# Kernel tuning notes

Measured on AMD Instinct MI355X. Metric: run time of the kernel, lower is better.

The kernel has to match this reference:

```python
import jax, jax.numpy as jnp
import numpy as np

N_NODES = 50000
N_EDGES = 800000
IN_SIZE = 128
NUM_HEADS = 8
HEAD_DIM = IN_SIZE // NUM_HEADS  # qk/val head dim = 16


def setup_inputs() -> dict:
    key = jax.random.key(0)
    ks = jax.random.split(key, 16)
    d = IN_SIZE
    lim = 1.0 / np.sqrt(d)
    inp = {
        "in_feats": jax.random.normal(ks[0], (N_NODES, d), jnp.float32),
        "struc_feats": jax.random.normal(ks[1], (N_NODES, d), jnp.float32),
        "edge_weights": jax.random.uniform(ks[2], (N_EDGES,), jnp.float32),
        "ln_scale": jnp.ones((d,), jnp.float32),
        "ln_bias": jnp.zeros((d,), jnp.float32),
        "Ws": jax.random.uniform(ks[3], (d, d), jnp.float32, -lim, lim),
        "bs": jnp.zeros((d,), jnp.float32),
        "Wq": jax.random.uniform(ks[4], (d, d), jnp.float32, -lim, lim),
        "bq": jnp.zeros((d,), jnp.float32),
        "Wk": jax.random.uniform(ks[5], (d, d), jnp.float32, -lim, lim),
        "bk": jnp.zeros((d,), jnp.float32),
        "Wv": jax.random.uniform(ks[6], (d, d), jnp.float32, -lim, lim),
        "bv": jnp.zeros((d,), jnp.float32),
        "Wo": jax.random.uniform(ks[7], (d, d), jnp.float32, -lim, lim),
        "edge_ids": jax.random.randint(ks[8], (2, N_EDGES), 0, N_NODES, jnp.int64)
        if jax.config.jax_enable_x64 else jax.random.randint(ks[8], (2, N_EDGES), 0, N_NODES, jnp.int32),
    }
    return inp


def _layer_norm(x, scale, bias, eps=1e-5):
    mu = jnp.mean(x, axis=-1, keepdims=True)
    var = jnp.var(x, axis=-1, keepdims=True)
    return (x - mu) * jax.lax.rsqrt(var + eps) * scale + bias


def reference(in_feats, struc_feats, edge_weights, ln_scale, ln_bias,
              Ws, bs, Wq, bq, Wk, bk, Wv, bv, Wo, edge_ids):
    N = in_feats.shape[0]
    H, hd = NUM_HEADS, HEAD_DIM

    delta = _layer_norm(in_feats, ln_scale, ln_bias)           # pre-norm
    delta = jax.nn.gelu(delta, approximate=False)               # pre-activation (exact GELU, torch default)
    delta_struc = delta + struc_feats @ Ws.T + bs               # struc_proj add

    qry = (delta_struc @ Wq.T + bq) / np.sqrt(hd)                # [N, qk]
    keyf = delta_struc @ Wk.T + bk                               # [N, qk]
    val = delta @ Wv.T + bv                                      # [N, val]

    src, dst = edge_ids[0], edge_ids[1]                          # out[src] += A[src,dst] * val[dst]
    qe = qry[src].reshape(-1, H, hd)                             # [E, H, hd]
    ke = keyf[dst].reshape(-1, H, hd)                            # [E, H, hd]
    attn = jax.nn.sigmoid(jnp.sum(qe * ke, axis=-1))             # [E, H]
    attn = edge_weights[:, None] * attn

    msgs = attn[:, :, None] * val[dst].reshape(-1, H, hd)        # [E, H, hd]
    agg = jax.ops.segment_sum(msgs.reshape(-1, H * hd), src, num_segments=N)  # [N, val]

    out = agg @ Wo.T                                             # out_proj (no bias)
    return in_feats + out                                        # skip connection
```

## Files before the change

### kernel.cpp

```cpp
#include <hip/hip_runtime.h>
#include <math.h>

#define NF 128

typedef __attribute__((ext_vector_type(8))) short short8;
typedef __attribute__((ext_vector_type(4))) float floatx4;

__device__ __forceinline__ unsigned short f2bf(float f) {
    union { float x; unsigned int i; } c; c.x = f;
    unsigned int r = c.i + 0x7fffu + ((c.i >> 16) & 1u);
    return (unsigned short)(r >> 16);
}
__device__ __forceinline__ float bf2f(unsigned short u) {
    union { unsigned int i; float x; } c; c.i = ((unsigned int)u) << 16;
    return c.x;
}
__device__ __forceinline__ void unpack8(uint4 u, float* f) {
    union { unsigned int i; float x; } c;
    c.i = u.x << 16;          f[0] = c.x;
    c.i = u.x & 0xffff0000u;  f[1] = c.x;
    c.i = u.y << 16;          f[2] = c.x;
    c.i = u.y & 0xffff0000u;  f[3] = c.x;
    c.i = u.z << 16;          f[4] = c.x;
    c.i = u.z & 0xffff0000u;  f[5] = c.x;
    c.i = u.w << 16;          f[6] = c.x;
    c.i = u.w & 0xffff0000u;  f[7] = c.x;
}
__device__ __forceinline__ ushort4 pack4(float a, float b, float c, float d) {
    ushort4 h; h.x = f2bf(a); h.y = f2bf(b); h.z = f2bf(c); h.w = f2bf(d);
    return h;
}

__global__ __launch_bounds__(256) void wconv_hist_kernel(
    const float* __restrict__ a, const float* __restrict__ b,
    const float* __restrict__ c, const float* __restrict__ d,
    const float* __restrict__ e, unsigned short* __restrict__ o,
    const int* __restrict__ eid, int* __restrict__ cnt,
    int* __restrict__ rank, int E)
{
    int blk = blockIdx.x;
    if (blk < 320) {
        int i = blk * 256 + threadIdx.x;
        int w = i >> 14, j = i & 16383;
        const float* p = (w == 0) ? a : (w == 1) ? b : (w == 2) ? c : (w == 3) ? d : e;
        o[i] = f2bf(p[j]);
    } else {
        int i = (blk - 320) * 256 + threadIdx.x;
        if (i < E) rank[i] = atomicAdd(&cnt[eid[i]], 1);
    }
}

__global__ __launch_bounds__(256) void scan1_kernel(
    const int* __restrict__ cnt, int* __restrict__ bsum, int n)
{
    int base = blockIdx.x * 1024;
    int s = 0;
    #pragma unroll
    for (int p = 0; p < 4; ++p) {
        int i = base + (int)threadIdx.x + p * 256;
        if (i < n) s += cnt[i];
    }
    #pragma unroll
    for (int m = 1; m <= 32; m <<= 1) s += __shfl_xor(s, m, 64);
    __shared__ int ws_[4];
    int wid = threadIdx.x >> 6;
    if ((threadIdx.x & 63) == 0) ws_[wid] = s;
    __syncthreads();
    if (threadIdx.x == 0) bsum[blockIdx.x] = ws_[0] + ws_[1] + ws_[2] + ws_[3];
}

__global__ __launch_bounds__(256) void scan3_kernel(
    const int* __restrict__ cnt, const int* __restrict__ bsum,
    int* __restrict__ row_start, int n, int nb)
{
    __shared__ int base_off;
    int tid = threadIdx.x, lane = tid & 63, wid = tid >> 6;
    if (tid == 0) {
        int a = 0;
        for (int j = 0; j < (int)blockIdx.x; ++j) a += bsum[j];
        base_off = a;
        if ((int)blockIdx.x == nb - 1) {
            int tot = a;
            for (int j = blockIdx.x; j < nb; ++j) tot += bsum[j];
            row_start[n] = tot;
        }
    }
    int base = blockIdx.x * 1024;
    int v[4]; int s = 0;
    #pragma unroll
    for (int p = 0; p < 4; ++p) {
        int i = base + tid * 4 + p;
        v[p] = (i < n) ? cnt[i] : 0;
        s += v[p];
    }
    int ss = s;
    #pragma unroll
    for (int off = 1; off < 64; off <<= 1) {
        int t = __shfl_up(ss, off, 64);
        if (lane >= off) ss += t;
    }
    __shared__ int wsum[4];
    if (lane == 63) wsum[wid] = ss;
    __syncthreads();
    int woff = 0;
    for (int j = 0; j < wid; ++j) woff += wsum[j];
    int a = base_off + woff + (ss - s);
    #pragma unroll
    for (int p = 0; p < 4; ++p) {
        int i = base + tid * 4 + p;
        if (i < n) { row_start[i] = a; a += v[p]; }
    }
}

__global__ __launch_bounds__(256) void scatter_prep_kernel(
    const int* __restrict__ eid, const float* __restrict__ ew,
    const int* __restrict__ row_start, const int* __restrict__ rank,
    int2* __restrict__ edata, int E, int sb,
    const float* __restrict__ in_feats, const float* __restrict__ gamma,
    const float* __restrict__ beta, unsigned short* __restrict__ deltab, int M)
{
    int blk = blockIdx.x;
    if (blk < sb) {
        int i = blk * 256 + threadIdx.x;
        if (i < E) {
            int src = eid[i];
            int pos = row_start[src] + rank[i];
            edata[pos] = make_int2(eid[E + i], __float_as_int(ew[i]));
        }
        return;
    }
    int li = (blk - sb) * 256 + threadIdx.x;
    int row = li >> 2, t4 = li & 3;
    if (row >= M) return;
    size_t rbase = (size_t)row * NF;

    const float4* ip = (const float4*)(in_feats + rbase) + t4 * 8;
    float4 xf[8];
    #pragma unroll
    for (int p = 0; p < 8; ++p) xf[p] = ip[p];
    float s = 0.f, sq = 0.f;
    #pragma unroll
    for (int p = 0; p < 8; ++p) {
        s  += xf[p].x + xf[p].y + xf[p].z + xf[p].w;
        sq += xf[p].x * xf[p].x + xf[p].y * xf[p].y
            + xf[p].z * xf[p].z + xf[p].w * xf[p].w;
    }
    s  += __shfl_xor(s, 1, 64);  s  += __shfl_xor(s, 2, 64);
    sq += __shfl_xor(sq, 1, 64); sq += __shfl_xor(sq, 2, 64);
    float mu = s * (1.0f / 128.0f);
    float var = sq * (1.0f / 128.0f) - mu * mu;
    float rstd = rsqrtf(var + 1e-5f);

    const float4* gp = (const float4*)gamma + t4 * 8;
    const float4* bp = (const float4*)beta + t4 * 8;
    uint dreg[16];
    #pragma unroll
    for (int p = 0; p < 8; ++p) {
        float4 g4 = gp[p], b4 = bp[p];
        float o0 = (xf[p].x - mu) * rstd * g4.x + b4.x;
        float o1 = (xf[p].y - mu) * rstd * g4.y + b4.y;
        float o2 = (xf[p].z - mu) * rstd * g4.z + b4.z;
        float o3 = (xf[p].w - mu) * rstd * g4.w + b4.w;
        o0 = 0.5f * o0 * (1.0f + erff(o0 * 0.70710678118654752f));
        o1 = 0.5f * o1 * (1.0f + erff(o1 * 0.70710678118654752f));
        o2 = 0.5f * o2 * (1.0f + erff(o2 * 0.70710678118654752f));
        o3 = 0.5f * o3 * (1.0f + erff(o3 * 0.70710678118654752f));
        ushort4 h = pack4(o0, o1, o2, o3);
        dreg[p * 2]     = (uint)h.x | ((uint)h.y << 16);
        dreg[p * 2 + 1] = (uint)h.z | ((uint)h.w << 16);
    }
    uint4* od = (uint4*)(deltab + rbase + t4 * 32);
    #pragma unroll
    for (int q = 0; q < 4; ++q)
        od[q] = make_uint4(dreg[q*4], dreg[q*4+1], dreg[q*4+2], dreg[q*4+3]);
}

__global__ __launch_bounds__(256) void gemm_dv_kernel(
    const float* __restrict__ struc, const unsigned short* __restrict__ deltab,
    const unsigned short* __restrict__ Wall, const float* __restrict__ bs,
    const float* __restrict__ bv, unsigned short* __restrict__ dstrb,
    unsigned short* __restrict__ kvb, int M, int nt)
{
    __shared__ unsigned short Wl[128][136];
    __shared__ unsigned short Cst[64][136];

    int tid = threadIdx.x;
    int y = blockIdx.y;
    int lane = tid & 63, w = tid >> 6, lg = lane & 15, quad = lane >> 4;

    const unsigned short* Wg = Wall + ((y == 0) ? 0 : 3 * 16384);
    const float* bias = (y == 0) ? bs : bv;
    unsigned short* outg = (y == 0) ? dstrb : (kvb + NF);
    int ostride = (y == 0) ? NF : 2 * NF;

    {
        const uint4* g = (const uint4*)Wg;
        #pragma unroll
        for (int p = 0; p < 8; ++p) {
            int idx = tid + p * 256;
            *(uint4*)&Wl[idx >> 4][(idx & 15) * 8] = g[idx];
        }
    }
    float br[8];
    #pragma unroll
    for (int t = 0; t < 8; ++t) br[t] = bias[t * 16 + lg];
    __syncthreads();

    for (int tile = blockIdx.x; tile < nt; tile += gridDim.x) {
        int m0 = tile * 64;
        int am = m0 + w * 16 + lg;
        size_t rb = (size_t)(am < M ? am : 0) * NF;

        short8 af[4];
        if (y == 0) {
            const float4* sp = (const float4*)(struc + rb);
            #pragma unroll
            for (int ks = 0; ks < 4; ++ks) {
                float4 f0 = sp[ks * 8 + quad * 2];
                float4 f1 = sp[ks * 8 + quad * 2 + 1];
                ushort4 h0 = pack4(f0.x, f0.y, f0.z, f0.w);
                ushort4 h1 = pack4(f1.x, f1.y, f1.z, f1.w);
                uint4 pk = make_uint4((uint)h0.x | ((uint)h0.y << 16),
                                      (uint)h0.z | ((uint)h0.w << 16),
                                      (uint)h1.x | ((uint)h1.y << 16),
                                      (uint)h1.z | ((uint)h1.w << 16));
                af[ks] = *(short8*)&pk;
            }
        } else {
            const unsigned short* arow = deltab + rb + quad * 8;
            #pragma unroll
            for (int ks = 0; ks < 4; ++ks) af[ks] = *(const short8*)(arow + ks * 32);
        }

        floatx4 acc[8];
        #pragma unroll
        for (int t = 0; t < 8; ++t) acc[t] = (floatx4){0.f, 0.f, 0.f, 0.f};
        #pragma unroll
        for (int ks = 0; ks < 4; ++ks) {
            #pragma unroll
            for (int t = 0; t < 8; ++t) {
                short8 b = *(const short8*)&Wl[t * 16 + lg][ks * 32 + quad * 8];
                acc[t] = __builtin_amdgcn_mfma_f32_16x16x32_bf16(af[ks], b, acc[t], 0, 0, 0);
            }
        }

        if (y == 0) {
            #pragma unroll
            for (int t = 0; t < 8; ++t) {
                int col = t * 16 + lg;
                #pragma unroll
                for (int r = 0; r < 4; ++r) {
                    int gm = m0 + w * 16 + quad * 4 + r;
                    float dadd = bf2f(deltab[(size_t)(gm < M ? gm : 0) * NF + col]);
                    Cst[w * 16 + quad * 4 + r][col] = f2bf(acc[t][r] + br[t] + dadd);
                }
            }
        } else {
            #pragma unroll
            for (int t = 0; t < 8; ++t) {
                int col = t * 16 + lg;
                #pragma unroll
                for (int r = 0; r < 4; ++r)
                    Cst[w * 16 + quad * 4 + r][col] = f2bf(acc[t][r] + br[t]);
            }
        }
        #pragma unroll
        for (int p = 0; p < 4; ++p) {
            int idx = lane + p * 64;
            int row = w * 16 + (idx >> 4), c16 = idx & 15;
            int gm = m0 + row;
            if (gm < M)
                *(uint4*)(outg + (size_t)gm * ostride + c16 * 8) = *(const uint4*)&Cst[row][c16 * 8];
        }
    }
}

__global__ __launch_bounds__(256) void gemm_qk_kernel(
    const unsigned short* __restrict__ dstrb, const unsigned short* __restrict__ Wall,
    const float* __restrict__ bq, const float* __restrict__ bk,
    unsigned short* __restrict__ qb, unsigned short* __restrict__ kvb,
    int M, int nt)
{
    __shared__ unsigned short Wl[128][136];
    __shared__ unsigned short Cst[64][136];

    int tid = threadIdx.x;
    int y = blockIdx.y;
    int lane = tid & 63, w = tid >> 6, lg = lane & 15, quad = lane >> 4;

    const unsigned short* Wg = Wall + (y + 1) * 16384;
    const float* bias = (y == 0) ? bq : bk;
    float scale = (y == 0) ? 0.25f : 1.0f;
    unsigned short* outg = (y == 0) ? qb : kvb;
    int ostride = (y == 0) ? NF : 2 * NF;

    {
        const uint4* g = (const uint4*)Wg;
        #pragma unroll
        for (int p = 0; p < 8; ++p) {
            int idx = tid + p * 256;
            *(uint4*)&Wl[idx >> 4][(idx & 15) * 8] = g[idx];
        }
    }
    float br[8];
    #pragma unroll
    for (int t = 0; t < 8; ++t) br[t] = bias[t * 16 + lg] * scale;
    __syncthreads();

    for (int tile = blockIdx.x; tile < nt; tile += gridDim.x) {
        int m0 = tile * 64;
        int am = m0 + w * 16 + lg;
        const unsigned short* arow = dstrb + (size_t)(am < M ? am : 0) * NF + quad * 8;

        floatx4 acc[8];
        #pragma unroll
        for (int t = 0; t < 8; ++t) acc[t] = (floatx4){0.f, 0.f, 0.f, 0.f};
        short8 af[4];
        #pragma unroll
        for (int ks = 0; ks < 4; ++ks) af[ks] = *(const short8*)(arow + ks * 32);
        #pragma unroll
        for (int ks = 0; ks < 4; ++ks) {
            #pragma unroll
            for (int t = 0; t < 8; ++t) {
                short8 b = *(const short8*)&Wl[t * 16 + lg][ks * 32 + quad * 8];
                acc[t] = __builtin_amdgcn_mfma_f32_16x16x32_bf16(af[ks], b, acc[t], 0, 0, 0);
            }
        }
        #pragma unroll
        for (int t = 0; t < 8; ++t) {
            int col = t * 16 + lg;
            #pragma unroll
            for (int r = 0; r < 4; ++r)
                Cst[w * 16 + quad * 4 + r][col] = f2bf(acc[t][r] * scale + br[t]);
        }
        #pragma unroll
        for (int p = 0; p < 4; ++p) {
            int idx = lane + p * 64;
            int row = w * 16 + (idx >> 4), c16 = idx & 15;
            int gm = m0 + row;
            if (gm < M)
                *(uint4*)(outg + (size_t)gm * ostride + c16 * 8) = *(const uint4*)&Cst[row][c16 * 8];
        }
    }
}

__global__ __launch_bounds__(256) void gemm_out_kernel(
    const unsigned short* __restrict__ Xb, const unsigned short* __restrict__ Wb,
    const float* __restrict__ addf, float* __restrict__ Y, int M, int nt)
{
    __shared__ unsigned short Wl[128][136];
    int tid = threadIdx.x;
    int lane = tid & 63, w = tid >> 6, lg = lane & 15, quad = lane >> 4;

    {
        const uint4* g = (const uint4*)Wb;
        #pragma unroll
        for (int p = 0; p < 8; ++p) {
            int idx = tid + p * 256;
            *(uint4*)&Wl[idx >> 4][(idx & 15) * 8] = g[idx];
        }
    }
    __syncthreads();

    for (int tile = blockIdx.x; tile < nt; tile += gridDim.x) {
        int m0 = tile * 64;
        int am = m0 + w * 16 + lg;
        const unsigned short* arow = Xb + (size_t)(am < M ? am : 0) * NF + quad * 8;

        floatx4 acc[8];
        #pragma unroll
        for (int t = 0; t < 8; ++t) acc[t] = (floatx4){0.f, 0.f, 0.f, 0.f};
        short8 af[4];
        #pragma unroll
        for (int ks = 0; ks < 4; ++ks) af[ks] = *(const short8*)(arow + ks * 32);
        #pragma unroll
        for (int ks = 0; ks < 4; ++ks) {
            #pragma unroll
            for (int t = 0; t < 8; ++t) {
                short8 b = *(const short8*)&Wl[t * 16 + lg][ks * 32 + quad * 8];
                acc[t] = __builtin_amdgcn_mfma_f32_16x16x32_bf16(af[ks], b, acc[t], 0, 0, 0);
            }
        }
        #pragma unroll
        for (int t = 0; t < 8; ++t) {
            int col = t * 16 + lg;
            #pragma unroll
            for (int r = 0; r < 4; ++r) {
                int gm = m0 + w * 16 + quad * 4 + r;
                if (gm >= M) continue;
                size_t off = (size_t)gm * NF + col;
                Y[off] = acc[t][r] + addf[off];
            }
        }
    }
}

__global__ __launch_bounds__(256) void aggregate_kernel(
    const unsigned short* __restrict__ Q, const unsigned short* __restrict__ kvb,
    const int* __restrict__ row_start, const int2* __restrict__ edata,
    unsigned short* __restrict__ agg, int N)
{
    int node = blockIdx.x * 4 + (threadIdx.x >> 6);
    if (node >= N) return;
    int lane = threadIdx.x & 63;
    int sg = lane >> 4, lg = lane & 15;
    int rs = row_start[node], re = row_start[node + 1];

    float qv[8];
    unpack8(*(const uint4*)(Q + (size_t)node * NF + lg * 8), qv);
    float acc[8];
    #pragma unroll
    for (int j = 0; j < 8; ++j) acc[j] = 0.f;

    int e1 = rs + sg, e2 = rs + sg + 4;
    int2 ed1 = (e1 < re) ? edata[e1] : make_int2(0, 0);
    int2 ed2 = (e2 < re) ? edata[e2] : make_int2(0, 0);

    for (int e0 = rs; e0 < re; e0 += 8) {
        int2 c1 = ed1, c2 = ed2;
        int en1 = e0 + 8 + sg, en2 = en1 + 4;
        ed1 = (en1 < re) ? edata[en1] : make_int2(0, 0);
        ed2 = (en2 < re) ? edata[en2] : make_int2(0, 0);

        const uint4* p1 = (const uint4*)kvb + (size_t)c1.x * 32 + lg;
        const uint4* p2 = (const uint4*)kvb + (size_t)c2.x * 32 + lg;
        uint4 k1u = p1[0], v1u = p1[16];
        uint4 k2u = p2[0], v2u = p2[16];

        float kv1[8], kv2[8];
        unpack8(k1u, kv1);
        unpack8(k2u, kv2);
        float s1 = qv[0] * kv1[0], s2 = qv[0] * kv2[0];
        #pragma unroll
        for (int j = 1; j < 8; ++j) {
            s1 = fmaf(qv[j], kv1[j], s1);
            s2 = fmaf(qv[j], kv2[j], s2);
        }
        s1 += __shfl_xor(s1, 1, 64);
        s2 += __shfl_xor(s2, 1, 64);
        float a1 = __int_as_float(c1.y) / (1.f + __expf(-s1));
        float a2 = __int_as_float(c2.y) / (1.f + __expf(-s2));

        float vv1[8], vv2[8];
        unpack8(v1u, vv1);
        unpack8(v2u, vv2);
        #pragma unroll
        for (int j = 0; j < 8; ++j) {
            acc[j] = fmaf(a1, vv1[j], acc[j]);
            acc[j] = fmaf(a2, vv2[j], acc[j]);
        }
    }
    #pragma unroll
    for (int j = 0; j < 8; ++j) {
        acc[j] += __shfl_xor(acc[j], 16, 64);
        acc[j] += __shfl_xor(acc[j], 32, 64);
    }
    if (sg == 0) {
        unsigned short* o = agg + (size_t)node * NF + lg * 8;
        *(ushort4*)o       = pack4(acc[0], acc[1], acc[2], acc[3]);
        *(ushort4*)(o + 4) = pack4(acc[4], acc[5], acc[6], acc[7]);
    }
}

extern "C" void kernel_launch(void* const* d_in, const int* in_sizes, int n_in,
                              void* d_out, int out_size, void* d_ws, size_t ws_size,
                              hipStream_t stream)
{
    const float* in_feats = (const float*)d_in[0];
    const float* struc    = (const float*)d_in[1];
    const float* eweights = (const float*)d_in[2];
    const float* ln_scale = (const float*)d_in[3];
    const float* ln_bias  = (const float*)d_in[4];
    const float* Ws       = (const float*)d_in[5];
    const float* bs       = (const float*)d_in[6];
    const float* Wq       = (const float*)d_in[7];
    const float* bq       = (const float*)d_in[8];
    const float* Wk       = (const float*)d_in[9];
    const float* bk       = (const float*)d_in[10];
    const float* Wv       = (const float*)d_in[11];
    const float* bv       = (const float*)d_in[12];
    const float* Wo       = (const float*)d_in[13];
    const int*   edge_ids = (const int*)d_in[14];
    float* out = (float*)d_out;

    int N = in_sizes[0] / NF;
    int E = in_sizes[2];

    size_t F = (size_t)N * NF;
    unsigned short* deltab = (unsigned short*)d_ws;
    unsigned short* dstrb  = deltab + F;
    unsigned short* qb     = dstrb + F;
    unsigned short* kvb    = qb + F;
    unsigned short* aggb   = kvb + 2 * F;
    unsigned short* Wall   = aggb + F;
    int2*  edata     = (int2*)(Wall + 5 * 16384);
    int*   cnt       = (int*)(edata + E);
    int*   row_start = cnt + N;
    int*   bsum      = row_start + N + 1;
    int*   rank      = bsum + 64;

    int nt  = (N + 63) / 64;
    int geb = (E + 255) / 256;
    int nb  = (N + 1023) / 1024;
    int ppb = (N * 4 + 255) / 256;

    hipMemsetAsync(cnt, 0, (size_t)N * sizeof(int), stream);
    wconv_hist_kernel<<<320 + geb, 256, 0, stream>>>(Ws, Wq, Wk, Wv, Wo, Wall,
                                                     edge_ids, cnt, rank, E);

    scan1_kernel<<<nb, 256, 0, stream>>>(cnt, bsum, N);
    scan3_kernel<<<nb, 256, 0, stream>>>(cnt, bsum, row_start, N, nb);

    scatter_prep_kernel<<<geb + ppb, 256, 0, stream>>>(edge_ids, eweights,
                                                       row_start, rank, edata, E, geb,
                                                       in_feats, ln_scale, ln_bias,
                                                       deltab, N);

    gemm_dv_kernel<<<dim3(261, 2), 256, 0, stream>>>(struc, deltab, Wall,
                                                     bs, bv, dstrb, kvb, N, nt);
    gemm_qk_kernel<<<dim3(261, 2), 256, 0, stream>>>(dstrb, Wall, bq, bk,
                                                     qb, kvb, N, nt);

    aggregate_kernel<<<(N + 3) / 4, 256, 0, stream>>>(qb, kvb, row_start, edata, aggb, N);

    gemm_out_kernel<<<nt, 256, 0, stream>>>(aggb, Wall + 4 * 16384, in_feats, out, N, nt);
}
```

Baseline: 292.6 us.

## Regroup prefix scan with layernorm and edge scatter with delta/value GEMM

Redistributes independent work across kernel launches. The scan3 pass is merged with the layernorm+GELU prep into one launch, and the edge scatter into CSR is merged with the struc/value GEMM into another. This cuts one kernel launch and lets the memory-bound scatter overlap with the GEMM tiles in the same grid. The trade-off is that scatter blocks now share a launch with blocks that allocate large shared memory, which may change occupancy and scheduling.

```diff
diff --git a/kernel.cpp b/kernel.cpp
--- a/kernel.cpp
+++ b/kernel.cpp
@@ -69,67 +69,54 @@
     if (threadIdx.x == 0) bsum[blockIdx.x] = ws_[0] + ws_[1] + ws_[2] + ws_[3];
 }
 
-__global__ __launch_bounds__(256) void scan3_kernel(
+__global__ __launch_bounds__(256) void scan3_ln_kernel(
     const int* __restrict__ cnt, const int* __restrict__ bsum,
-    int* __restrict__ row_start, int n, int nb)
-{
-    __shared__ int base_off;
-    int tid = threadIdx.x, lane = tid & 63, wid = tid >> 6;
-    if (tid == 0) {
-        int a = 0;
-        for (int j = 0; j < (int)blockIdx.x; ++j) a += bsum[j];
-        base_off = a;
-        if ((int)blockIdx.x == nb - 1) {
-            int tot = a;
-            for (int j = blockIdx.x; j < nb; ++j) tot += bsum[j];
-            row_start[n] = tot;
-        }
-    }
-    int base = blockIdx.x * 1024;
-    int v[4]; int s = 0;
-    #pragma unroll
-    for (int p = 0; p < 4; ++p) {
-        int i = base + tid * 4 + p;
-        v[p] = (i < n) ? cnt[i] : 0;
-        s += v[p];
-    }
-    int ss = s;
-    #pragma unroll
-    for (int off = 1; off < 64; off <<= 1) {
-        int t = __shfl_up(ss, off, 64);
-        if (lane >= off) ss += t;
-    }
-    __shared__ int wsum[4];
-    if (lane == 63) wsum[wid] = ss;
-    __syncthreads();
-    int woff = 0;
-    for (int j = 0; j < wid; ++j) woff += wsum[j];
-    int a = base_off + woff + (ss - s);
-    #pragma unroll
-    for (int p = 0; p < 4; ++p) {
-        int i = base + tid * 4 + p;
-        if (i < n) { row_start[i] = a; a += v[p]; }
-    }
-}
-
-__global__ __launch_bounds__(256) void scatter_prep_kernel(
-    const int* __restrict__ eid, const float* __restrict__ ew,
-    const int* __restrict__ row_start, const int* __restrict__ rank,
-    int2* __restrict__ edata, int E, int sb,
+    int* __restrict__ row_start, int n, int nb,
     const float* __restrict__ in_feats, const float* __restrict__ gamma,
     const float* __restrict__ beta, unsigned short* __restrict__ deltab, int M)
 {
     int blk = blockIdx.x;
-    if (blk < sb) {
-        int i = blk * 256 + threadIdx.x;
-        if (i < E) {
-            int src = eid[i];
-            int pos = row_start[src] + rank[i];
-            edata[pos] = make_int2(eid[E + i], __float_as_int(ew[i]));
+    if (blk < nb) {
+        __shared__ int base_off;
+        int tid = threadIdx.x, lane = tid & 63, wid = tid >> 6;
+        if (tid == 0) {
+            int a = 0;
+            for (int j = 0; j < blk; ++j) a += bsum[j];
+            base_off = a;
+            if (blk == nb - 1) {
+                int tot = a;
+                for (int j = blk; j < nb; ++j) tot += bsum[j];
+                row_start[n] = tot;
+            }
+        }
+        int base = blk * 1024;
+        int v[4]; int s = 0;
+        #pragma unroll
+        for (int p = 0; p < 4; ++p) {
+            int i = base + tid * 4 + p;
+            v[p] = (i < n) ? cnt[i] : 0;
+            s += v[p];
+        }
+        int ss = s;
+        #pragma unroll
+        for (int off = 1; off < 64; off <<= 1) {
+            int t = __shfl_up(ss, off, 64);
+            if (lane >= off) ss += t;
+        }
+        __shared__ int wsum[4];
+        if (lane == 63) wsum[wid] = ss;
+        __syncthreads();
+        int woff = 0;
+        for (int j = 0; j < wid; ++j) woff += wsum[j];
+        int a = base_off + woff + (ss - s);
+        #pragma unroll
+        for (int p = 0; p < 4; ++p) {
+            int i = base + tid * 4 + p;
+            if (i < n) { row_start[i] = a; a += v[p]; }
         }
         return;
     }
-    int li = (blk - sb) * 256 + threadIdx.x;
+    int li = (blk - nb) * 256 + threadIdx.x;
     int row = li >> 2, t4 = li & 3;
     if (row >= M) return;
     size_t rbase = (size_t)row * NF;
@@ -175,17 +162,34 @@
         od[q] = make_uint4(dreg[q*4], dreg[q*4+1], dreg[q*4+2], dreg[q*4+3]);
 }
 
-__global__ __launch_bounds__(256) void gemm_dv_kernel(
+__global__ __launch_bounds__(256) void scatter_dv_kernel(
+    const int* __restrict__ eid, const float* __restrict__ ew,
+    const int* __restrict__ row_start, const int* __restrict__ rank,
+    int2* __restrict__ edata, int E, int sb,
     const float* __restrict__ struc, const unsigned short* __restrict__ deltab,
     const unsigned short* __restrict__ Wall, const float* __restrict__ bs,
     const float* __restrict__ bv, unsigned short* __restrict__ dstrb,
-    unsigned short* __restrict__ kvb, int M, int nt)
+    unsigned short* __restrict__ kvb, int M, int nt, int ndv)
 {
     __shared__ unsigned short Wl[128][136];
     __shared__ unsigned short Cst[64][136];
 
+    int blk = blockIdx.x;
+    if (blk < sb) {
+        int i = blk * 256 + threadIdx.x;
+        if (i < E) {
+            int src = eid[i];
+            int pos = row_start[src] + rank[i];
+            edata[pos] = make_int2(eid[E + i], __float_as_int(ew[i]));
+        }
+        return;
+    }
+
+    int idx = blk - sb;
+    int y = idx / ndv;
+    int xb = idx % ndv;
+
     int tid = threadIdx.x;
-    int y = blockIdx.y;
     int lane = tid & 63, w = tid >> 6, lg = lane & 15, quad = lane >> 4;
 
     const unsigned short* Wg = Wall + ((y == 0) ? 0 : 3 * 16384);
@@ -197,8 +201,8 @@
         const uint4* g = (const uint4*)Wg;
         #pragma unroll
         for (int p = 0; p < 8; ++p) {
-            int idx = tid + p * 256;
-            *(uint4*)&Wl[idx >> 4][(idx & 15) * 8] = g[idx];
+            int i2 = tid + p * 256;
+            *(uint4*)&Wl[i2 >> 4][(i2 & 15) * 8] = g[i2];
         }
     }
     float br[8];
@@ -206,7 +210,7 @@
     for (int t = 0; t < 8; ++t) br[t] = bias[t * 16 + lg];
     __syncthreads();
 
-    for (int tile = blockIdx.x; tile < nt; tile += gridDim.x) {
+    for (int tile = xb; tile < nt; tile += ndv) {
         int m0 = tile * 64;
         int am = m0 + w * 16 + lg;
         size_t rb = (size_t)(am < M ? am : 0) * NF;
@@ -266,8 +270,8 @@
         }
         #pragma unroll
         for (int p = 0; p < 4; ++p) {
-            int idx = lane + p * 64;
-            int row = w * 16 + (idx >> 4), c16 = idx & 15;
+            int i2 = lane + p * 64;
+            int row = w * 16 + (i2 >> 4), c16 = i2 & 15;
             int gm = m0 + row;
             if (gm < M)
                 *(uint4*)(outg + (size_t)gm * ostride + c16 * 8) = *(const uint4*)&Cst[row][c16 * 8];
@@ -503,21 +507,23 @@
     int geb = (E + 255) / 256;
     int nb  = (N + 1023) / 1024;
     int ppb = (N * 4 + 255) / 256;
+    int ndv = 261;
 
     hipMemsetAsync(cnt, 0, (size_t)N * sizeof(int), stream);
     wconv_hist_kernel<<<320 + geb, 256, 0, stream>>>(Ws, Wq, Wk, Wv, Wo, Wall,
                                                      edge_ids, cnt, rank, E);
 
     scan1_kernel<<<nb, 256, 0, stream>>>(cnt, bsum, N);
-    scan3_kernel<<<nb, 256, 0, stream>>>(cnt, bsum, row_start, N, nb);
-
-    scatter_prep_kernel<<<geb + ppb, 256, 0, stream>>>(edge_ids, eweights,
-                                                       row_start, rank, edata, E, geb,
-                                                       in_feats, ln_scale, ln_bias,
-                                                       deltab, N);
-
-    gemm_dv_kernel<<<dim3(261, 2), 256, 0, stream>>>(struc, deltab, Wall,
-                                                     bs, bv, dstrb, kvb, N, nt);
+
+    scan3_ln_kernel<<<nb + ppb, 256, 0, stream>>>(cnt, bsum, row_start, N, nb,
+                                                  in_feats, ln_scale, ln_bias,
+                                                  deltab, N);
+
+    scatter_dv_kernel<<<geb + 2 * ndv, 256, 0, stream>>>(edge_ids, eweights,
+                                                         row_start, rank, edata, E, geb,
+                                                         struc, deltab, Wall, bs, bv,
+                                                         dstrb, kvb, N, nt, ndv);
+
     gemm_qk_kernel<<<dim3(261, 2), 256, 0, stream>>>(dstrb, Wall, bq, bk,
                                                      qb, kvb, N, nt);
 
```

New measurement: 290.6 us. No clear change (-0.7%).
